# Optimization experiments

Hardware: AMD Instinct MI355X
Metric: run time of the kernel (lower is better)

The kernel has to match this reference:

```python
import jax, jax.numpy as jnp
import numpy as np

NB_CLASSES = 100000
SZ_EMBED = 64
SZ_BATCH = 1024


def setup_inputs() -> dict:
    key = jax.random.key(0)
    k1, k2, k3 = jax.random.split(key, 3)
    xs = jax.random.normal(k1, (SZ_BATCH, SZ_EMBED), dtype=jnp.float32)
    ys = jax.random.randint(k2, (SZ_BATCH,), 0, NB_CLASSES, dtype=jnp.int64)
    # xavier_uniform for an Embedding(nb_classes, sz_embed)
    limit = float(np.sqrt(6.0 / (NB_CLASSES + SZ_EMBED)))
    proxies = jax.random.uniform(k3, (NB_CLASSES, SZ_EMBED), dtype=jnp.float32,
                                 minval=-limit, maxval=limit)
    return {"xs": xs, "ys": ys, "proxies": proxies}


def reference(xs, ys, proxies):
    # L2-normalize each proxy row (torch F.normalize; eps guard like torch's 1e-12).
    # Note: the original normalizes the positive proxy with dim=0 on a 1-D vector,
    # which is identical to per-row normalization.
    norms = jnp.linalg.norm(proxies, axis=1, keepdims=True)
    P = proxies / jnp.maximum(norms, 1e-12)                      # [C, D]

    # Squared euclidean distance matrix D[i, c] = ||x_i - P_c||^2 via GEMM
    x_sq = jnp.sum(xs * xs, axis=1, keepdims=True)               # [B, 1]
    p_sq = jnp.sum(P * P, axis=1)                                # [C]
    dist = jnp.maximum(x_sq + p_sq[None, :] - 2.0 * (xs @ P.T), 0.0)  # [B, C]

    logits = -dist                                               # [B, C]
    ys = ys.astype(jnp.int32)
    d_pos = jnp.take_along_axis(dist, ys[:, None], axis=1)[:, 0]  # [B]

    # log sum over negatives (c != y) of exp(-dist)
    neg_mask = jnp.arange(NB_CLASSES)[None, :] != ys[:, None]    # [B, C]
    neg_logits = jnp.where(neg_mask, logits, -jnp.inf)
    log_n = jax.nn.logsumexp(neg_logits, axis=1)                 # [B]

    # -log(p / n) = dist_pos + log(sum_neg exp(-dist))
    per_sample = d_pos + log_n
    return jnp.mean(per_sample)
```

## Files before the change

### kernel.cpp

```cpp
#include <hip/hip_runtime.h>
#include <math.h>

#define B 1024
#define C 100000
#define D 64
#define TC 128
#define NCH 782
#define NPADROWS (NCH * TC)
#define CPAD (NPADROWS - C)
#define NP NCH
#define L2E 1.4426950408889634f

typedef __attribute__((ext_vector_type(8))) short short8;
typedef __attribute__((ext_vector_type(4))) float f32x4;

#define WS_PART 0
#define WS_CW2  ((size_t)NCH * B * 4)
#define WS_XBF  (WS_CW2 + B * 4)

#define GLB(p) ((const __attribute__((address_space(1))) void*)(p))
#define LDS(p) ((__attribute__((address_space(3))) void*)(p))

static __device__ __forceinline__ unsigned short f2bf(float f) {
    unsigned u = __float_as_uint(f);
    return (unsigned short)((u + 0x7fffu + ((u >> 16) & 1u)) >> 16);
}
static __device__ __forceinline__ float bf_round(float f) {
    return __uint_as_float(((unsigned)f2bf(f)) << 16);
}
static __device__ __forceinline__ float fexp2(float x) {
#if __has_builtin(__builtin_amdgcn_exp2f)
    return __builtin_amdgcn_exp2f(x);
#else
    return __expf(x * 0.6931471805599453f);
#endif
}

__global__ __launch_bounds__(256) void proxynca_prepx(
    const float* __restrict__ xs, unsigned short* __restrict__ Xbf,
    float* __restrict__ cw2)
{
    const int t = threadIdx.x;
    const int rl = t >> 4, f4 = t & 15;
    const int row = blockIdx.x * 16 + rl;
    const float4 v = *(const float4*)(xs + (size_t)row * D + f4 * 4);
    float ss = v.x*v.x + v.y*v.y + v.z*v.z + v.w*v.w;
    ss += __shfl_xor(ss, 1); ss += __shfl_xor(ss, 2);
    ss += __shfl_xor(ss, 4); ss += __shfl_xor(ss, 8);
    ushort4 w;
    w.x = f2bf(v.x); w.y = f2bf(v.y); w.z = f2bf(v.z); w.w = f2bf(v.w);
    *(ushort4*)(Xbf + (size_t)row * D + f4 * 4) = w;
    if (f4 == 0) cw2[row] = -2.0f * sqrtf(ss) * L2E;
}

__global__ __launch_bounds__(512, 4) void proxynca_main(
    const float* __restrict__ proxies, const unsigned short* __restrict__ Xbf,
    const float* __restrict__ cw2v, float* __restrict__ partial)
{
    __shared__ __align__(16) unsigned short Ash[256 * 64];
    __shared__ __align__(16) unsigned short Bsh[TC * 64];
    __shared__ float crow[256];
    __shared__ __align__(8) float scratch[256][2];

    const int t = threadIdx.x;
    const int lane = t & 63;
    const int wv = t >> 6;
    const int rg = blockIdx.x;
    const int ct = blockIdx.y;
    const int rbase = rg * 256;

    const unsigned short* Asrc = Xbf + (size_t)rbase * D;

    #pragma unroll
    for (int j = 0; j < 4; ++j) {
        int c = (j * 8 + wv) * 64 + lane;
        int row = c >> 3, q = c & 7;
        int sc = (row << 3) | (q ^ (row & 7));
        __builtin_amdgcn_global_load_lds(GLB(Asrc + sc * 8),
            LDS(Ash + (size_t)(j * 8 + wv) * 512), 16, 0, 0);
    }

    #pragma unroll
    for (int i = 0; i < 4; ++i) {
        int idx = i * 512 + t;
        int r = idx >> 4, f4 = idx & 15;
        int gc = ct * TC + r;
        float4 v = make_float4(0.f, 0.f, 0.f, 0.f);
        if (gc < C) v = *(const float4*)(proxies + (size_t)gc * D + f4 * 4);
        float ss = v.x*v.x + v.y*v.y + v.z*v.z + v.w*v.w;
        ss += __shfl_xor(ss, 1); ss += __shfl_xor(ss, 2);
        ss += __shfl_xor(ss, 4); ss += __shfl_xor(ss, 8);
        float rn = 1.0f / fmaxf(sqrtf(ss), 1e-12f);
        ushort4 w;
        w.x = f2bf(v.x * rn); w.y = f2bf(v.y * rn);
        w.z = f2bf(v.z * rn); w.w = f2bf(v.w * rn);
        int p = (f4 >> 1) ^ (r & 7);
        *(ushort4*)(Bsh + (size_t)((r * 8 + p) * 8 + (f4 & 1) * 4)) = w;
    }
    if (t < 256) crow[t] = cw2v[rbase + t];
    __syncthreads();

    const int quad = lane >> 4, sixt = lane & 15;
    const int mg = wv >> 1;
    const int ng = wv & 1;

    short8 bfr[4][2];
    #pragma unroll
    for (int ns = 0; ns < 4; ++ns) {
        int cl = ng * 64 + ns * 16 + sixt;
        int sw = cl & 7;
        bfr[ns][0] = *(const short8*)(Bsh + (size_t)(((cl << 3) | (quad ^ sw)) * 8));
        bfr[ns][1] = *(const short8*)(Bsh + (size_t)(((cl << 3) | ((4 + quad) ^ sw)) * 8));
    }
    short8 af[4][2];
    #pragma unroll
    for (int ms = 0; ms < 4; ++ms) {
        int rowL = mg * 64 + ms * 16 + sixt;
        int sw = rowL & 7;
        af[ms][0] = *(const short8*)(Ash + (size_t)(((rowL << 3) | (quad ^ sw)) * 8));
        af[ms][1] = *(const short8*)(Ash + (size_t)(((rowL << 3) | ((4 + quad) ^ sw)) * 8));
    }
    float cw[4][4];
    #pragma unroll
    for (int ms = 0; ms < 4; ++ms)
        #pragma unroll
        for (int rgi = 0; rgi < 4; ++rgi)
            cw[ms][rgi] = crow[mg * 64 + ms * 16 + quad * 4 + rgi];

    float s_acc[4][4];
    #pragma unroll
    for (int ms = 0; ms < 4; ++ms)
        #pragma unroll
        for (int rgi = 0; rgi < 4; ++rgi) s_acc[ms][rgi] = 0.f;

    #pragma unroll
    for (int ns = 0; ns < 4; ++ns)
        #pragma unroll
        for (int ms = 0; ms < 4; ++ms) {
            f32x4 acc = {0.f, 0.f, 0.f, 0.f};
            acc = __builtin_amdgcn_mfma_f32_16x16x32_bf16(af[ms][0], bfr[ns][0], acc, 0, 0, 0);
            acc = __builtin_amdgcn_mfma_f32_16x16x32_bf16(af[ms][1], bfr[ns][1], acc, 0, 0, 0);
            #pragma unroll
            for (int rgi = 0; rgi < 4; ++rgi)
                s_acc[ms][rgi] += fexp2(fmaf(2.0f * L2E, acc[rgi], cw[ms][rgi]));
        }

    #pragma unroll
    for (int ms = 0; ms < 4; ++ms)
        #pragma unroll
        for (int rgi = 0; rgi < 4; ++rgi) {
            float s = s_acc[ms][rgi];
            s += __shfl_xor(s, 1); s += __shfl_xor(s, 2);
            s += __shfl_xor(s, 4); s += __shfl_xor(s, 8);
            if (sixt == 0)
                scratch[mg * 64 + ms * 16 + quad * 4 + rgi][ng] = s;
        }
    __syncthreads();
    if (t < 256)
        partial[(size_t)ct * B + rbase + t] = scratch[t][0] + scratch[t][1];
}

__global__ __launch_bounds__(256) void proxynca_reduce(
    const float* __restrict__ xs, const int* __restrict__ ys,
    const float* __restrict__ proxies, const float* __restrict__ partial,
    float* __restrict__ out)
{
    __shared__ float acc4[4];
    const int lane = threadIdx.x & 63;
    const int w = threadIdx.x >> 6;
    const int row = blockIdx.x * 4 + w;

    float x = xs[(size_t)row * D + lane];
    int y = ys[row];
    float p = proxies[(size_t)y * D + lane];

    float xx = x * x, pp = p * p;
    #pragma unroll
    for (int off = 1; off < 64; off <<= 1) {
        xx += __shfl_xor(xx, off);
        pp += __shfl_xor(pp, off);
    }
    float nx = sqrtf(xx);
    float rn = 1.0f / fmaxf(sqrtf(pp), 1e-12f);
    float ph = p * rn;

    float xp = x * ph;
    float xpb = bf_round(x) * bf_round(ph);
    #pragma unroll
    for (int off = 1; off < 64; off <<= 1) {
        xp  += __shfl_xor(xp, off);
        xpb += __shfl_xor(xpb, off);
    }

    float s = 0.f;
    for (int j = lane; j < NP; j += 64) s += partial[(size_t)j * B + row];
    #pragma unroll
    for (int off = 1; off < 64; off <<= 1) s += __shfl_xor(s, off);

    if (lane == 0) {
        float cw2r = -2.0f * nx * L2E;
        float e_pos = fexp2(fmaf(2.0f * L2E, xpb, cw2r));
        float e_pad = fexp2(cw2r);
        float s_neg = s - e_pos - (float)CPAD * e_pad;
        acc4[w] = 2.0f * (nx - xp) + logf(s_neg);
    }
    __syncthreads();
    if (threadIdx.x == 0) {
        float v = acc4[0] + acc4[1] + acc4[2] + acc4[3];
        atomicAdd(out, v * (1.0f / (float)B));
    }
}

extern "C" void kernel_launch(void* const* d_in, const int* in_sizes, int n_in,
                              void* d_out, int out_size, void* d_ws, size_t ws_size,
                              hipStream_t stream)
{
    const float* xs      = (const float*)d_in[0];
    const int*   ys      = (const int*)d_in[1];
    const float* proxies = (const float*)d_in[2];
    char* ws = (char*)d_ws;
    float* partial = (float*)(ws + WS_PART);
    float* cw2     = (float*)(ws + WS_CW2);
    unsigned short* Xbf = (unsigned short*)(ws + WS_XBF);
    float* out = (float*)d_out;

    hipMemsetAsync(out, 0, sizeof(float), stream);
    proxynca_prepx<<<B / 16, 256, 0, stream>>>(xs, Xbf, cw2);
    dim3 gridA(4, NCH);
    proxynca_main<<<gridA, 512, 0, stream>>>(proxies, Xbf, cw2, partial);
    proxynca_reduce<<<B / 4, 256, 0, stream>>>(xs, ys, proxies, partial, out);
}
```

Baseline: 132.6 us.

## Pre-normalize proxies to bf16 once, async-load tiles, add split row-sum kernel

Proxy normalization and bf16 conversion move out of the main GEMM kernel into a merged prep kernel that writes a padded bf16 proxy buffer. The main kernel then loads both tiles straight into LDS with async global-to-LDS copies instead of four redundant fp32 loads plus normalization in each of the 4 row-group blocks. The cross-lane reduction is cut to one shuffle, with the result staged into the reused B tile, and the occupancy hint drops from 4 to 3 blocks. A separate column-sum kernel replaces the strided per-row partial read inside the final reduce. This costs an extra pass writing and reading about 12.8 MB of bf16 proxies plus one more launch.

```diff
diff --git a/kernel.cpp b/kernel.cpp
--- a/kernel.cpp
+++ b/kernel.cpp
@@ -8,7 +8,6 @@
 #define NCH 782
 #define NPADROWS (NCH * TC)
 #define CPAD (NPADROWS - C)
-#define NP NCH
 #define L2E 1.4426950408889634f
 
 typedef __attribute__((ext_vector_type(8))) short short8;
@@ -17,6 +16,8 @@
 #define WS_PART 0
 #define WS_CW2  ((size_t)NCH * B * 4)
 #define WS_XBF  (WS_CW2 + B * 4)
+#define WS_PBF  (WS_XBF + (size_t)B * D * 2)
+#define WS_RSUM (WS_PBF + (size_t)NPADROWS * D * 2)
 
 #define GLB(p) ((const __attribute__((address_space(1))) void*)(p))
 #define LDS(p) ((__attribute__((address_space(3))) void*)(p))
@@ -36,57 +37,18 @@
 #endif
 }
 
-__global__ __launch_bounds__(256) void proxynca_prepx(
-    const float* __restrict__ xs, unsigned short* __restrict__ Xbf,
+__global__ __launch_bounds__(256) void proxynca_prep(
+    const float* __restrict__ xs, const float* __restrict__ proxies,
+    unsigned short* __restrict__ Xbf, unsigned short* __restrict__ Pbf,
     float* __restrict__ cw2)
 {
     const int t = threadIdx.x;
     const int rl = t >> 4, f4 = t & 15;
-    const int row = blockIdx.x * 16 + rl;
-    const float4 v = *(const float4*)(xs + (size_t)row * D + f4 * 4);
-    float ss = v.x*v.x + v.y*v.y + v.z*v.z + v.w*v.w;
-    ss += __shfl_xor(ss, 1); ss += __shfl_xor(ss, 2);
-    ss += __shfl_xor(ss, 4); ss += __shfl_xor(ss, 8);
-    ushort4 w;
-    w.x = f2bf(v.x); w.y = f2bf(v.y); w.z = f2bf(v.z); w.w = f2bf(v.w);
-    *(ushort4*)(Xbf + (size_t)row * D + f4 * 4) = w;
-    if (f4 == 0) cw2[row] = -2.0f * sqrtf(ss) * L2E;
-}
-
-__global__ __launch_bounds__(512, 4) void proxynca_main(
-    const float* __restrict__ proxies, const unsigned short* __restrict__ Xbf,
-    const float* __restrict__ cw2v, float* __restrict__ partial)
-{
-    __shared__ __align__(16) unsigned short Ash[256 * 64];
-    __shared__ __align__(16) unsigned short Bsh[TC * 64];
-    __shared__ float crow[256];
-    __shared__ __align__(8) float scratch[256][2];
-
-    const int t = threadIdx.x;
-    const int lane = t & 63;
-    const int wv = t >> 6;
-    const int rg = blockIdx.x;
-    const int ct = blockIdx.y;
-    const int rbase = rg * 256;
-
-    const unsigned short* Asrc = Xbf + (size_t)rbase * D;
-
-    #pragma unroll
-    for (int j = 0; j < 4; ++j) {
-        int c = (j * 8 + wv) * 64 + lane;
-        int row = c >> 3, q = c & 7;
-        int sc = (row << 3) | (q ^ (row & 7));
-        __builtin_amdgcn_global_load_lds(GLB(Asrc + sc * 8),
-            LDS(Ash + (size_t)(j * 8 + wv) * 512), 16, 0, 0);
-    }
-
-    #pragma unroll
-    for (int i = 0; i < 4; ++i) {
-        int idx = i * 512 + t;
-        int r = idx >> 4, f4 = idx & 15;
-        int gc = ct * TC + r;
+    const int bb = blockIdx.x;
+    if (bb < NPADROWS / 16) {
+        int gr = bb * 16 + rl;
         float4 v = make_float4(0.f, 0.f, 0.f, 0.f);
-        if (gc < C) v = *(const float4*)(proxies + (size_t)gc * D + f4 * 4);
+        if (gr < C) v = *(const float4*)(proxies + (size_t)gr * D + f4 * 4);
         float ss = v.x*v.x + v.y*v.y + v.z*v.z + v.w*v.w;
         ss += __shfl_xor(ss, 1); ss += __shfl_xor(ss, 2);
         ss += __shfl_xor(ss, 4); ss += __shfl_xor(ss, 8);
@@ -94,8 +56,52 @@
         ushort4 w;
         w.x = f2bf(v.x * rn); w.y = f2bf(v.y * rn);
         w.z = f2bf(v.z * rn); w.w = f2bf(v.w * rn);
-        int p = (f4 >> 1) ^ (r & 7);
-        *(ushort4*)(Bsh + (size_t)((r * 8 + p) * 8 + (f4 & 1) * 4)) = w;
+        *(ushort4*)(Pbf + (size_t)gr * D + f4 * 4) = w;
+    } else {
+        int row = (bb - NPADROWS / 16) * 16 + rl;
+        const float4 v = *(const float4*)(xs + (size_t)row * D + f4 * 4);
+        float ss = v.x*v.x + v.y*v.y + v.z*v.z + v.w*v.w;
+        ss += __shfl_xor(ss, 1); ss += __shfl_xor(ss, 2);
+        ss += __shfl_xor(ss, 4); ss += __shfl_xor(ss, 8);
+        ushort4 w;
+        w.x = f2bf(v.x); w.y = f2bf(v.y); w.z = f2bf(v.z); w.w = f2bf(v.w);
+        *(ushort4*)(Xbf + (size_t)row * D + f4 * 4) = w;
+        if (f4 == 0) cw2[row] = -2.0f * sqrtf(ss) * L2E;
+    }
+}
+
+__global__ __launch_bounds__(512, 3) void proxynca_main(
+    const unsigned short* __restrict__ Pbf, const unsigned short* __restrict__ Xbf,
+    const float* __restrict__ cw2v, float* __restrict__ partial)
+{
+    __shared__ __align__(16) unsigned short Ash[256 * 64];
+    __shared__ __align__(16) unsigned short Bsh[TC * 64];
+    __shared__ float crow[256];
+
+    const int t = threadIdx.x;
+    const int lane = t & 63;
+    const int wv = t >> 6;
+    const int rg = blockIdx.x;
+    const int ct = blockIdx.y;
+    const int rbase = rg * 256;
+
+    const unsigned short* Asrc = Xbf + (size_t)rbase * D;
+    #pragma unroll
+    for (int j = 0; j < 4; ++j) {
+        int c = (j * 8 + wv) * 64 + lane;
+        int row = c >> 3, p = c & 7;
+        int sc = (row << 3) | (p ^ (row & 7));
+        __builtin_amdgcn_global_load_lds(GLB(Asrc + sc * 8),
+            LDS(Ash + (size_t)(j * 8 + wv) * 512), 16, 0, 0);
+    }
+    const unsigned short* Bsrc = Pbf + (size_t)ct * TC * D;
+    #pragma unroll
+    for (int j = 0; j < 2; ++j) {
+        int c = (j * 8 + wv) * 64 + lane;
+        int row = c >> 3, p = c & 7;
+        int sc = (row << 3) | (p ^ (row & 7));
+        __builtin_amdgcn_global_load_lds(GLB(Bsrc + sc * 8),
+            LDS(Bsh + (size_t)(j * 8 + wv) * 512), 16, 0, 0);
     }
     if (t < 256) crow[t] = cw2v[rbase + t];
     __syncthreads();
@@ -120,6 +126,8 @@
         af[ms][0] = *(const short8*)(Ash + (size_t)(((rowL << 3) | (quad ^ sw)) * 8));
         af[ms][1] = *(const short8*)(Ash + (size_t)(((rowL << 3) | ((4 + quad) ^ sw)) * 8));
     }
+    __syncthreads();
+
     float cw[4][4];
     #pragma unroll
     for (int ms = 0; ms < 4; ++ms)
@@ -145,24 +153,51 @@
                 s_acc[ms][rgi] += fexp2(fmaf(2.0f * L2E, acc[rgi], cw[ms][rgi]));
         }
 
+    float (*scratch)[16] = (float(*)[16])Bsh;
     #pragma unroll
     for (int ms = 0; ms < 4; ++ms)
         #pragma unroll
         for (int rgi = 0; rgi < 4; ++rgi) {
-            float s = s_acc[ms][rgi];
-            s += __shfl_xor(s, 1); s += __shfl_xor(s, 2);
-            s += __shfl_xor(s, 4); s += __shfl_xor(s, 8);
-            if (sixt == 0)
-                scratch[mg * 64 + ms * 16 + quad * 4 + rgi][ng] = s;
+            float s = s_acc[ms][rgi] + __shfl_xor(s_acc[ms][rgi], 1);
+            if ((sixt & 1) == 0)
+                scratch[mg * 64 + ms * 16 + quad * 4 + rgi][ng * 8 + (sixt >> 1)] = s;
         }
     __syncthreads();
-    if (t < 256)
-        partial[(size_t)ct * B + rbase + t] = scratch[t][0] + scratch[t][1];
+    if (t < 256) {
+        const float* r = scratch[t];
+        float4 a = *(const float4*)(r);
+        float4 b = *(const float4*)(r + 4);
+        float4 c = *(const float4*)(r + 8);
+        float4 d = *(const float4*)(r + 12);
+        float s = ((a.x + a.y) + (a.z + a.w)) + ((b.x + b.y) + (b.z + b.w))
+                + ((c.x + c.y) + (c.z + c.w)) + ((d.x + d.y) + (d.z + d.w));
+        partial[(size_t)ct * B + rbase + t] = s;
+    }
+}
+
+__global__ __launch_bounds__(256) void proxynca_sumk(
+    const float* __restrict__ partial, float* __restrict__ rowsum)
+{
+    __shared__ float red[32][8];
+    const int t = threadIdx.x;
+    const int rl = t & 31;
+    const int pp = t >> 5;
+    const int row = blockIdx.x * 32 + rl;
+    float s = 0.f;
+    for (int j = pp; j < NCH; j += 8)
+        s += partial[(size_t)j * B + row];
+    red[rl][pp] = s;
+    __syncthreads();
+    if (t < 32) {
+        const float* r = red[t];
+        rowsum[blockIdx.x * 32 + t] =
+            ((r[0] + r[1]) + (r[2] + r[3])) + ((r[4] + r[5]) + (r[6] + r[7]));
+    }
 }
 
 __global__ __launch_bounds__(256) void proxynca_reduce(
     const float* __restrict__ xs, const int* __restrict__ ys,
-    const float* __restrict__ proxies, const float* __restrict__ partial,
+    const float* __restrict__ proxies, const float* __restrict__ rowsum,
     float* __restrict__ out)
 {
     __shared__ float acc4[4];
@@ -192,12 +227,8 @@
         xpb += __shfl_xor(xpb, off);
     }
 
-    float s = 0.f;
-    for (int j = lane; j < NP; j += 64) s += partial[(size_t)j * B + row];
-    #pragma unroll
-    for (int off = 1; off < 64; off <<= 1) s += __shfl_xor(s, off);
-
     if (lane == 0) {
+        float s = rowsum[row];
         float cw2r = -2.0f * nx * L2E;
         float e_pos = fexp2(fmaf(2.0f * L2E, xpb, cw2r));
         float e_pad = fexp2(cw2r);
@@ -222,11 +253,14 @@
     float* partial = (float*)(ws + WS_PART);
     float* cw2     = (float*)(ws + WS_CW2);
     unsigned short* Xbf = (unsigned short*)(ws + WS_XBF);
+    unsigned short* Pbf = (unsigned short*)(ws + WS_PBF);
+    float* rowsum  = (float*)(ws + WS_RSUM);
     float* out = (float*)d_out;
 
     hipMemsetAsync(out, 0, sizeof(float), stream);
-    proxynca_prepx<<<B / 16, 256, 0, stream>>>(xs, Xbf, cw2);
+    proxynca_prep<<<NPADROWS / 16 + B / 16, 256, 0, stream>>>(xs, proxies, Xbf, Pbf, cw2);
     dim3 gridA(4, NCH);
-    proxynca_main<<<gridA, 512, 0, stream>>>(proxies, Xbf, cw2, partial);
-    proxynca_reduce<<<B / 4, 256, 0, stream>>>(xs, ys, proxies, partial, out);
-}
+    proxynca_main<<<gridA, 512, 0, stream>>>(Pbf, Xbf, cw2, partial);
+    proxynca_sumk<<<B / 32, 256, 0, stream>>>(partial, rowsum);
+    proxynca_reduce<<<B / 4, 256, 0, stream>>>(xs, ys, proxies, rowsum, out);
+}
```

Measured after the change: 142.2 us. 7.2% more time.

## Loop over all batch row tiles per block to reuse normalized proxy tile

Applied to the files above, without the earlier changes.

Each block now handles one proxy chunk and loops over all four 256-row batch tiles, so each proxy tile is loaded and normalized once instead of four times. The next X tile is prefetched into LDS while the current tile's MFMA work runs. The LDS cross-wave reduction is replaced by writing per-wave-column partials into two planes with vector stores. The reduce kernel is restructured to sum both planes with coalesced loads over 32 rows per block. The costs are a serialized loop with extra barriers, fewer blocks (782), and twice the partial buffer traffic.

```diff
diff --git a/kernel.cpp b/kernel.cpp
--- a/kernel.cpp
+++ b/kernel.cpp
@@ -8,14 +8,13 @@
 #define NCH 782
 #define NPADROWS (NCH * TC)
 #define CPAD (NPADROWS - C)
-#define NP NCH
 #define L2E 1.4426950408889634f
 
 typedef __attribute__((ext_vector_type(8))) short short8;
 typedef __attribute__((ext_vector_type(4))) float f32x4;
 
 #define WS_PART 0
-#define WS_CW2  ((size_t)NCH * B * 4)
+#define WS_CW2  ((size_t)2 * NCH * B * 4)
 #define WS_XBF  (WS_CW2 + B * 4)
 
 #define GLB(p) ((const __attribute__((address_space(1))) void*)(p))
@@ -53,33 +52,27 @@
     if (f4 == 0) cw2[row] = -2.0f * sqrtf(ss) * L2E;
 }
 
-__global__ __launch_bounds__(512, 4) void proxynca_main(
+__global__ __launch_bounds__(512, 6) void proxynca_main(
     const float* __restrict__ proxies, const unsigned short* __restrict__ Xbf,
     const float* __restrict__ cw2v, float* __restrict__ partial)
 {
     __shared__ __align__(16) unsigned short Ash[256 * 64];
     __shared__ __align__(16) unsigned short Bsh[TC * 64];
-    __shared__ float crow[256];
-    __shared__ __align__(8) float scratch[256][2];
+    __shared__ __align__(16) float crow[B];
 
     const int t = threadIdx.x;
     const int lane = t & 63;
     const int wv = t >> 6;
-    const int rg = blockIdx.x;
-    const int ct = blockIdx.y;
-    const int rbase = rg * 256;
-
-    const unsigned short* Asrc = Xbf + (size_t)rbase * D;
+    const int ct = blockIdx.x;
 
     #pragma unroll
     for (int j = 0; j < 4; ++j) {
         int c = (j * 8 + wv) * 64 + lane;
-        int row = c >> 3, q = c & 7;
-        int sc = (row << 3) | (q ^ (row & 7));
-        __builtin_amdgcn_global_load_lds(GLB(Asrc + sc * 8),
+        int row = c >> 3, p = c & 7;
+        int sc = (row << 3) | (p ^ (row & 7));
+        __builtin_amdgcn_global_load_lds(GLB(Xbf + sc * 8),
             LDS(Ash + (size_t)(j * 8 + wv) * 512), 16, 0, 0);
     }
-
     #pragma unroll
     for (int i = 0; i < 4; ++i) {
         int idx = i * 512 + t;
@@ -97,7 +90,8 @@
         int p = (f4 >> 1) ^ (r & 7);
         *(ushort4*)(Bsh + (size_t)((r * 8 + p) * 8 + (f4 & 1) * 4)) = w;
     }
-    if (t < 256) crow[t] = cw2v[rbase + t];
+    crow[t] = cw2v[t];
+    crow[t + 512] = cw2v[t + 512];
     __syncthreads();
 
     const int quad = lane >> 4, sixt = lane & 15;
@@ -112,52 +106,73 @@
         bfr[ns][0] = *(const short8*)(Bsh + (size_t)(((cl << 3) | (quad ^ sw)) * 8));
         bfr[ns][1] = *(const short8*)(Bsh + (size_t)(((cl << 3) | ((4 + quad) ^ sw)) * 8));
     }
-    short8 af[4][2];
-    #pragma unroll
-    for (int ms = 0; ms < 4; ++ms) {
-        int rowL = mg * 64 + ms * 16 + sixt;
-        int sw = rowL & 7;
-        af[ms][0] = *(const short8*)(Ash + (size_t)(((rowL << 3) | (quad ^ sw)) * 8));
-        af[ms][1] = *(const short8*)(Ash + (size_t)(((rowL << 3) | ((4 + quad) ^ sw)) * 8));
-    }
-    float cw[4][4];
-    #pragma unroll
-    for (int ms = 0; ms < 4; ++ms)
-        #pragma unroll
-        for (int rgi = 0; rgi < 4; ++rgi)
-            cw[ms][rgi] = crow[mg * 64 + ms * 16 + quad * 4 + rgi];
-
-    float s_acc[4][4];
-    #pragma unroll
-    for (int ms = 0; ms < 4; ++ms)
-        #pragma unroll
-        for (int rgi = 0; rgi < 4; ++rgi) s_acc[ms][rgi] = 0.f;
-
-    #pragma unroll
-    for (int ns = 0; ns < 4; ++ns)
+
+    float* plane = partial + (size_t)ng * NCH * B + (size_t)ct * B;
+
+    for (int rt = 0; rt < 4; ++rt) {
+        short8 af[4][2];
         #pragma unroll
         for (int ms = 0; ms < 4; ++ms) {
-            f32x4 acc = {0.f, 0.f, 0.f, 0.f};
-            acc = __builtin_amdgcn_mfma_f32_16x16x32_bf16(af[ms][0], bfr[ns][0], acc, 0, 0, 0);
-            acc = __builtin_amdgcn_mfma_f32_16x16x32_bf16(af[ms][1], bfr[ns][1], acc, 0, 0, 0);
-            #pragma unroll
-            for (int rgi = 0; rgi < 4; ++rgi)
-                s_acc[ms][rgi] += fexp2(fmaf(2.0f * L2E, acc[rgi], cw[ms][rgi]));
-        }
-
-    #pragma unroll
-    for (int ms = 0; ms < 4; ++ms)
-        #pragma unroll
-        for (int rgi = 0; rgi < 4; ++rgi) {
-            float s = s_acc[ms][rgi];
-            s += __shfl_xor(s, 1); s += __shfl_xor(s, 2);
-            s += __shfl_xor(s, 4); s += __shfl_xor(s, 8);
-            if (sixt == 0)
-                scratch[mg * 64 + ms * 16 + quad * 4 + rgi][ng] = s;
-        }
-    __syncthreads();
-    if (t < 256)
-        partial[(size_t)ct * B + rbase + t] = scratch[t][0] + scratch[t][1];
+            int rowL = mg * 64 + ms * 16 + sixt;
+            int sw = rowL & 7;
+            af[ms][0] = *(const short8*)(Ash + (size_t)(((rowL << 3) | (quad ^ sw)) * 8));
+            af[ms][1] = *(const short8*)(Ash + (size_t)(((rowL << 3) | ((4 + quad) ^ sw)) * 8));
+        }
+        f32x4 cwv[4];
+        #pragma unroll
+        for (int ms = 0; ms < 4; ++ms)
+            cwv[ms] = *(const f32x4*)(crow + rt * 256 + mg * 64 + ms * 16 + quad * 4);
+
+        __syncthreads();
+
+        if (rt < 3) {
+            const unsigned short* An = Xbf + (size_t)(rt + 1) * 256 * D;
+            #pragma unroll
+            for (int j = 0; j < 4; ++j) {
+                int c = (j * 8 + wv) * 64 + lane;
+                int row = c >> 3, p = c & 7;
+                int sc = (row << 3) | (p ^ (row & 7));
+                __builtin_amdgcn_global_load_lds(GLB(An + sc * 8),
+                    LDS(Ash + (size_t)(j * 8 + wv) * 512), 16, 0, 0);
+            }
+        }
+
+        float s_acc[4][4];
+        #pragma unroll
+        for (int ms = 0; ms < 4; ++ms)
+            #pragma unroll
+            for (int rgi = 0; rgi < 4; ++rgi) s_acc[ms][rgi] = 0.f;
+
+        #pragma unroll
+        for (int ns = 0; ns < 4; ++ns)
+            #pragma unroll
+            for (int ms = 0; ms < 4; ++ms) {
+                f32x4 acc = {0.f, 0.f, 0.f, 0.f};
+                acc = __builtin_amdgcn_mfma_f32_16x16x32_bf16(af[ms][0], bfr[ns][0], acc, 0, 0, 0);
+                acc = __builtin_amdgcn_mfma_f32_16x16x32_bf16(af[ms][1], bfr[ns][1], acc, 0, 0, 0);
+                #pragma unroll
+                for (int rgi = 0; rgi < 4; ++rgi)
+                    s_acc[ms][rgi] += fexp2(fmaf(2.0f * L2E, acc[rgi], cwv[ms][rgi]));
+            }
+
+        #pragma unroll
+        for (int ms = 0; ms < 4; ++ms)
+            #pragma unroll
+            for (int rgi = 0; rgi < 4; ++rgi) {
+                float s = s_acc[ms][rgi];
+                s += __shfl_xor(s, 1); s += __shfl_xor(s, 2);
+                s += __shfl_xor(s, 4); s += __shfl_xor(s, 8);
+                s_acc[ms][rgi] = s;
+            }
+        if (sixt == 0) {
+            #pragma unroll
+            for (int ms = 0; ms < 4; ++ms) {
+                f32x4 v = {s_acc[ms][0], s_acc[ms][1], s_acc[ms][2], s_acc[ms][3]};
+                *(f32x4*)(plane + rt * 256 + mg * 64 + ms * 16 + quad * 4) = v;
+            }
+        }
+        __syncthreads();
+    }
 }
 
 __global__ __launch_bounds__(256) void proxynca_reduce(
@@ -165,50 +180,70 @@
     const float* __restrict__ proxies, const float* __restrict__ partial,
     float* __restrict__ out)
 {
-    __shared__ float acc4[4];
-    const int lane = threadIdx.x & 63;
-    const int w = threadIdx.x >> 6;
-    const int row = blockIdx.x * 4 + w;
-
-    float x = xs[(size_t)row * D + lane];
-    int y = ys[row];
-    float p = proxies[(size_t)y * D + lane];
-
-    float xx = x * x, pp = p * p;
-    #pragma unroll
-    for (int off = 1; off < 64; off <<= 1) {
-        xx += __shfl_xor(xx, off);
-        pp += __shfl_xor(pp, off);
-    }
-    float nx = sqrtf(xx);
-    float rn = 1.0f / fmaxf(sqrtf(pp), 1e-12f);
-    float ph = p * rn;
-
-    float xp = x * ph;
-    float xpb = bf_round(x) * bf_round(ph);
-    #pragma unroll
-    for (int off = 1; off < 64; off <<= 1) {
-        xp  += __shfl_xor(xp, off);
-        xpb += __shfl_xor(xpb, off);
-    }
-
-    float s = 0.f;
-    for (int j = lane; j < NP; j += 64) s += partial[(size_t)j * B + row];
-    #pragma unroll
-    for (int off = 1; off < 64; off <<= 1) s += __shfl_xor(s, off);
-
-    if (lane == 0) {
-        float cw2r = -2.0f * nx * L2E;
-        float e_pos = fexp2(fmaf(2.0f * L2E, xpb, cw2r));
-        float e_pad = fexp2(cw2r);
-        float s_neg = s - e_pos - (float)CPAD * e_pad;
-        acc4[w] = 2.0f * (nx - xp) + logf(s_neg);
-    }
-    __syncthreads();
-    if (threadIdx.x == 0) {
-        float v = acc4[0] + acc4[1] + acc4[2] + acc4[3];
-        atomicAdd(out, v * (1.0f / (float)B));
-    }
+    __shared__ float red[32][8];
+    __shared__ float rowsumL[32];
+    __shared__ float wacc[4];
+
+    const int t = threadIdx.x;
+    const int row0 = blockIdx.x * 32;
+    const float* pl0 = partial;
+    const float* pl1 = partial + (size_t)NCH * B;
+
+    {
+        const int rl = t & 31, pp = t >> 5;
+        float s = 0.f;
+        for (int j = pp; j < NCH; j += 8) {
+            size_t o = (size_t)j * B + row0 + rl;
+            s += pl0[o] + pl1[o];
+        }
+        red[rl][pp] = s;
+    }
+    __syncthreads();
+    if (t < 32) {
+        const float* r = red[t];
+        rowsumL[t] = ((r[0] + r[1]) + (r[2] + r[3])) + ((r[4] + r[5]) + (r[6] + r[7]));
+    }
+    __syncthreads();
+
+    const int lane = t & 63, w = t >> 6;
+    float myacc = 0.f;
+    for (int i = 0; i < 8; ++i) {
+        int rloc = w * 8 + i;
+        int row = row0 + rloc;
+        float x = xs[(size_t)row * D + lane];
+        int y = ys[row];
+        float p = proxies[(size_t)y * D + lane];
+
+        float xx = x * x, pq = p * p;
+        #pragma unroll
+        for (int off = 1; off < 64; off <<= 1) {
+            xx += __shfl_xor(xx, off);
+            pq += __shfl_xor(pq, off);
+        }
+        float nx = sqrtf(xx);
+        float rn = 1.0f / fmaxf(sqrtf(pq), 1e-12f);
+        float ph = p * rn;
+
+        float xp = x * ph;
+        float xpb = bf_round(x) * bf_round(ph);
+        #pragma unroll
+        for (int off = 1; off < 64; off <<= 1) {
+            xp  += __shfl_xor(xp, off);
+            xpb += __shfl_xor(xpb, off);
+        }
+        if (lane == 0) {
+            float s = rowsumL[rloc];
+            float cw2r = -2.0f * nx * L2E;
+            float e_pos = fexp2(fmaf(2.0f * L2E, xpb, cw2r));
+            float e_pad = fexp2(cw2r);
+            float s_neg = s - e_pos - (float)CPAD * e_pad;
+            myacc += 2.0f * (nx - xp) + logf(s_neg);
+        }
+    }
+    if (lane == 0) wacc[w] = myacc;
+    __syncthreads();
+    if (t == 0)
+        atomicAdd(out, (wacc[0] + wacc[1] + wacc[2] + wacc[3]) * (1.0f / (float)B));
 }
 
 extern "C" void kernel_launch(void* const* d_in, const int* in_sizes, int n_in,
@@ -226,7 +261,6 @@
 
     hipMemsetAsync(out, 0, sizeof(float), stream);
     proxynca_prepx<<<B / 16, 256, 0, stream>>>(xs, Xbf, cw2);
-    dim3 gridA(4, NCH);
-    proxynca_main<<<gridA, 512, 0, stream>>>(proxies, Xbf, cw2, partial);
-    proxynca_reduce<<<B / 4, 256, 0, stream>>>(xs, ys, proxies, partial, out);
-}
+    proxynca_main<<<NCH, 512, 0, stream>>>(proxies, Xbf, cw2, partial);
+    proxynca_reduce<<<B / 32, 256, 0, stream>>>(xs, ys, proxies, partial, out);
+}
```

After: 269.3 us. +103.1%, slower.
